# Optimization experiments

Hardware: AMD Instinct MI355X
Metric: run time of the kernel (lower is better)

## Reference

```python
import jax, jax.numpy as jnp
import numpy as np

B, M, HID, NH = 2, 2048, 1024, 16
D = HID // NH  # 64


def setup_inputs() -> dict:
    key = jax.random.key(0)
    ks = jax.random.split(key, 6)
    s = 0.02  # weight init scale
    return {
        "h": jax.random.normal(ks[0], (B, M, HID), dtype=jnp.float32),
        "key_pe": jax.random.normal(ks[1], (1, D, M), dtype=jnp.float32) * s,
        "Wq": jax.random.normal(ks[2], (HID, HID), dtype=jnp.float32) * s,
        "Wk": jax.random.normal(ks[3], (HID, HID), dtype=jnp.float32) * s,
        "Wv": jax.random.normal(ks[4], (HID, HID), dtype=jnp.float32) * s,
        "Wo": jax.random.normal(ks[5], (HID, HID), dtype=jnp.float32) * s,
    }


def reference(h, key_pe, Wq, Wk, Wv, Wo):
    # Faithful to the source: in SelfAttention.forward the gathered-span scores
    # are overwritten by dense Q K^T, and the softmaxed `attn` is discarded;
    # the returned value is (Q K^T) V (no scaling, no softmax). key_pe only
    # feeds the dead softmax branch, so it does not affect the output.
    b, m, hd = h.shape
    nh, d = NH, hd // NH

    def heads(x):  # (B, M, HID) -> (B, NH, M, D)
        return x.reshape(b, m, nh, d).transpose(0, 2, 1, 3)

    q = heads(h @ Wq.T)
    k = heads(h @ Wk.T)
    v = heads(h @ Wv.T)

    attn_cont = jnp.einsum("bhqd,bhkd->bhqk", q, k)  # (B, NH, M, M)
    out = jnp.einsum("bhqk,bhkd->bhqd", attn_cont, v)  # (B, NH, M, D)
    out = out.transpose(0, 2, 1, 3).reshape(b, m, hd)  # (B, M, HID)
    return out @ Wo.T
```

## Files before the change

### kernel.cpp

```cpp
#include <hip/hip_runtime.h>
#include <hip/hip_bf16.h>


typedef unsigned short u16;
typedef unsigned int u32;
typedef __attribute__((ext_vector_type(8))) short bf16x8;
typedef __attribute__((ext_vector_type(4))) float f32x4;

__device__ __forceinline__ void async_copy16(void* lds, const void* g) {
  __builtin_amdgcn_global_load_lds((const __attribute__((address_space(1))) void*)g,
                                   (__attribute__((address_space(3))) void*)lds,
                                   16, 0, 0);
}

__device__ __forceinline__ u16 f2bf(float f) {
  union { __hip_bfloat16 h; u16 u; } c;
  c.h = __float2bfloat16(f);
  return c.u;
}
__device__ __forceinline__ float bflo(u32 w) {
  union { u32 u; float f; } c; c.u = w << 16; return c.f;
}
__device__ __forceinline__ float bfhi(u32 w) {
  union { u32 u; float f; } c; c.u = w & 0xFFFF0000u; return c.f;
}
__device__ __forceinline__ ushort4 cvt4(float4 v) {
  ushort4 o; o.x = f2bf(v.x); o.y = f2bf(v.y); o.z = f2bf(v.z); o.w = f2bf(v.w);
  return o;
}

__global__ __launch_bounds__(256) void prep(const float4* __restrict__ h,
                                            const float4* __restrict__ wq,
                                            const float4* __restrict__ wk,
                                            const float4* __restrict__ wv,
                                            ushort4* __restrict__ hb,
                                            ushort4* __restrict__ wcat) {
  int i = blockIdx.x * 256 + threadIdx.x;
  if (i < 1048576) { hb[i] = cvt4(h[i]); return; }
  i -= 1048576;
  if (i < 262144) { wcat[i] = cvt4(wq[i]); return; }
  i -= 262144;
  if (i < 262144) { wcat[262144 + i] = cvt4(wk[i]); return; }
  i -= 262144;
  wcat[524288 + i] = cvt4(wv[i]);
}

template <bool BF16_OUT>
__global__ __launch_bounds__(256) void gemm_bt(const u16* __restrict__ A, int lda,
                                               const u16* __restrict__ B0,
                                               const u16* __restrict__ B1,
                                               void* __restrict__ Cv,
                                               int N, int K) {
  __shared__ u16 Als[128 * 64];
  __shared__ u16 Bls[128 * 64];
  const int t = threadIdx.x;
  const int lane = t & 63;
  const int wave = t >> 6;
  const int wm = (wave >> 1) * 64;
  const int wn = (wave & 1) * 64;
  const int lrow = lane & 15;
  const int quad = lane >> 4;
  const int m0 = blockIdx.y * 128;
  const int n0 = blockIdx.x * 128;
  const u16* B = (B1 != nullptr && m0 >= 2048) ? B1 : B0;

  const int srow = t >> 3;
  const int scol = (((t & 7) ^ (srow & 7)) * 8);
  const u16* Ag0 = A + (size_t)(m0 + srow) * lda + scol;
  const u16* Bg0 = B + (size_t)(n0 + srow) * K + scol;
  u16* Al0 = Als + t * 8;
  u16* Bl0 = Bls + t * 8;

  f32x4 acc[4][4];
#pragma unroll
  for (int i = 0; i < 4; ++i)
#pragma unroll
    for (int j = 0; j < 4; ++j) acc[i][j] = {0.f, 0.f, 0.f, 0.f};

  for (int k0 = 0; k0 < K; k0 += 64) {
#pragma unroll
    for (int c = 0; c < 4; ++c)
      async_copy16(Al0 + c * 2048, Ag0 + (size_t)(c * 32) * lda + k0);
#pragma unroll
    for (int c = 0; c < 4; ++c)
      async_copy16(Bl0 + c * 2048, Bg0 + (size_t)(c * 32) * K + k0);
    __syncthreads();

#pragma unroll
    for (int half = 0; half < 2; ++half) {
      const int gg = quad + half * 4;
      bf16x8 af[4], bfv[4];
#pragma unroll
      for (int i = 0; i < 4; ++i) {
        const int ra = wm + i * 16 + lrow;
        const int rb = wn + i * 16 + lrow;
        af[i]  = *(const bf16x8*)(Als + ra * 64 + ((gg ^ (ra & 7)) << 3));
        bfv[i] = *(const bf16x8*)(Bls + rb * 64 + ((gg ^ (rb & 7)) << 3));
      }
#pragma unroll
      for (int mi = 0; mi < 4; ++mi)
#pragma unroll
        for (int ni = 0; ni < 4; ++ni)
          acc[mi][ni] = __builtin_amdgcn_mfma_f32_16x16x32_bf16(
              af[mi], bfv[ni], acc[mi][ni], 0, 0, 0);
    }
    __syncthreads();
  }

  const int crow0 = m0 + wm + (lane >> 4) * 4;
  const int ccol0 = n0 + wn + (lane & 15);
#pragma unroll
  for (int mi = 0; mi < 4; ++mi)
#pragma unroll
    for (int ni = 0; ni < 4; ++ni) {
      const int col = ccol0 + ni * 16;
#pragma unroll
      for (int r = 0; r < 4; ++r) {
        const size_t idx = (size_t)(crow0 + mi * 16 + r) * N + col;
        if (BF16_OUT) ((u16*)Cv)[idx]   = f2bf(acc[mi][ni][r]);
        else          ((float*)Cv)[idx] = acc[mi][ni][r];
      }
    }
}

__global__ __launch_bounds__(256) void s_kernel(const u16* __restrict__ QKV,
                                                float* __restrict__ Spart) {
  const int bh = blockIdx.x;
  const int b = bh >> 4, hh = bh & 15;
  const int row0 = b * 2048 + blockIdx.y * 128;
  const u16* Kg = QKV + (size_t)row0 * 3072 + 1024 + hh * 64;

  __shared__ float Ks[64][64];
  __shared__ float Vs[64][64];
  const int t = threadIdx.x;
  const int lr = t >> 2;
  const int lc = (t & 3) * 16;
  const int d1 = (t >> 4) * 4;
  const int d2 = (t & 15) * 4;

  float acc[4][4] = {};

  for (int r0 = 0; r0 < 128; r0 += 64) {
    const u16* kp = Kg + (size_t)(r0 + lr) * 3072 + lc;
    const uint4 kw0 = *(const uint4*)kp;
    const uint4 kw1 = *(const uint4*)(kp + 8);
    const uint4 vw0 = *(const uint4*)(kp + 1024);
    const uint4 vw1 = *(const uint4*)(kp + 1032);
    __syncthreads();
    float* kd = &Ks[lr][lc];
    *(float4*)(kd)      = float4{bflo(kw0.x), bfhi(kw0.x), bflo(kw0.y), bfhi(kw0.y)};
    *(float4*)(kd + 4)  = float4{bflo(kw0.z), bfhi(kw0.z), bflo(kw0.w), bfhi(kw0.w)};
    *(float4*)(kd + 8)  = float4{bflo(kw1.x), bfhi(kw1.x), bflo(kw1.y), bfhi(kw1.y)};
    *(float4*)(kd + 12) = float4{bflo(kw1.z), bfhi(kw1.z), bflo(kw1.w), bfhi(kw1.w)};
    float* vd = &Vs[lr][lc];
    *(float4*)(vd)      = float4{bflo(vw0.x), bfhi(vw0.x), bflo(vw0.y), bfhi(vw0.y)};
    *(float4*)(vd + 4)  = float4{bflo(vw0.z), bfhi(vw0.z), bflo(vw0.w), bfhi(vw0.w)};
    *(float4*)(vd + 8)  = float4{bflo(vw1.x), bfhi(vw1.x), bflo(vw1.y), bfhi(vw1.y)};
    *(float4*)(vd + 12) = float4{bflo(vw1.z), bfhi(vw1.z), bflo(vw1.w), bfhi(vw1.w)};
    __syncthreads();
#pragma unroll
    for (int r = 0; r < 64; ++r) {
      float kv[4], vv[4];
      *(float4*)kv = *(const float4*)&Ks[r][d1];
      *(float4*)vv = *(const float4*)&Vs[r][d2];
#pragma unroll
      for (int i = 0; i < 4; ++i)
#pragma unroll
        for (int j = 0; j < 4; ++j) acc[i][j] += kv[i] * vv[j];
    }
  }
  float* Sp = Spart + ((size_t)bh * 16 + blockIdx.y) * 4096;
#pragma unroll
  for (int i = 0; i < 4; ++i)
    *(float4*)&Sp[(d1 + i) * 64 + d2] =
        float4{acc[i][0], acc[i][1], acc[i][2], acc[i][3]};
}

__global__ __launch_bounds__(256) void reduce_s(const float4* __restrict__ Spart,
                                                float4* __restrict__ S) {
  const int g = blockIdx.x * 256 + threadIdx.x;
  const int bh = g >> 10, j = g & 1023;
  const float4* p = Spart + (size_t)bh * 16384 + j;
  float4 a = {0.f, 0.f, 0.f, 0.f};
#pragma unroll
  for (int c = 0; c < 16; ++c) {
    const float4 v = p[(size_t)c * 1024];
    a.x += v.x; a.y += v.y; a.z += v.z; a.w += v.w;
  }
  S[g] = a;
}

__global__ __launch_bounds__(256) void t_kernel(const float* __restrict__ S,
                                                const float* __restrict__ Wo,
                                                u16* __restrict__ Tt) {
  const int n0 = blockIdx.x * 128;
  const int hh = blockIdx.y;
  const int b  = blockIdx.z;
  __shared__ float Ss[64][68];
  __shared__ float Ws[128][68];
  const int t = threadIdx.x;
  {
    const float* sg = S + (size_t)(b * 16 + hh) * 4096 + (t >> 2) * 64 + (t & 3) * 16;
    float* sd = &Ss[t >> 2][(t & 3) * 16];
#pragma unroll
    for (int i = 0; i < 4; ++i) *(float4*)(sd + 4 * i) = *(const float4*)(sg + 4 * i);
    const float* wg = Wo + (size_t)(n0 + (t >> 1)) * 1024 + hh * 64 + (t & 1) * 32;
    float* wd = &Ws[t >> 1][(t & 1) * 32];
#pragma unroll
    for (int i = 0; i < 8; ++i) *(float4*)(wd + 4 * i) = *(const float4*)(wg + 4 * i);
  }
  __syncthreads();

  const int td = (t >> 4) * 4;
  const int tn = t & 15;
  float acc[4][8] = {};
  for (int jj = 0; jj < 64; jj += 4) {
    float4 sv[4], wv[8];
#pragma unroll
    for (int i = 0; i < 4; ++i) sv[i] = *(const float4*)&Ss[td + i][jj];
#pragma unroll
    for (int k = 0; k < 8; ++k) wv[k] = *(const float4*)&Ws[tn + 16 * k][jj];
#pragma unroll
    for (int i = 0; i < 4; ++i)
#pragma unroll
      for (int k = 0; k < 8; ++k)
        acc[i][k] += sv[i].x * wv[k].x + sv[i].y * wv[k].y +
                     sv[i].z * wv[k].z + sv[i].w * wv[k].w;
  }

  u16* tp = Tt + (size_t)b * 1048576;
#pragma unroll
  for (int k = 0; k < 8; ++k) {
    const int n = n0 + tn + 16 * k;
    ushort4 o;
    o.x = f2bf(acc[0][k]); o.y = f2bf(acc[1][k]);
    o.z = f2bf(acc[2][k]); o.w = f2bf(acc[3][k]);
    *(ushort4*)&tp[(size_t)n * 1024 + hh * 64 + td] = o;
  }
}

extern "C" void kernel_launch(void* const* d_in, const int* in_sizes, int n_in,
                              void* d_out, int out_size, void* d_ws, size_t ws_size,
                              hipStream_t stream) {
  const float* h  = (const float*)d_in[0];
  const float* Wq = (const float*)d_in[2];
  const float* Wk = (const float*)d_in[3];
  const float* Wv = (const float*)d_in[4];
  const float* Wo = (const float*)d_in[5];

  char* ws = (char*)d_ws;
  u16*   hb    = (u16*)(ws);
  u16*   wcat  = (u16*)(ws + (8ull  << 20));
  u16*   QKVb  = (u16*)(ws + (16ull << 20));
  float* S     = (float*)(ws + (40ull << 20));
  u16*   Tt    = (u16*)(ws + (41ull << 20));
  float* Spart = (float*)(ws + (48ull << 20));

  prep<<<7168, 256, 0, stream>>>((const float4*)h, (const float4*)Wq,
                                 (const float4*)Wk, (const float4*)Wv,
                                 (ushort4*)hb, (ushort4*)wcat);
  gemm_bt<true><<<dim3(24, 32), 256, 0, stream>>>(hb, 1024, wcat, nullptr,
                                                  QKVb, 3072, 1024);
  s_kernel<<<dim3(32, 16), 256, 0, stream>>>(QKVb, Spart);
  reduce_s<<<128, 256, 0, stream>>>((const float4*)Spart, (float4*)S);
  t_kernel<<<dim3(8, 16, 2), 256, 0, stream>>>(S, Wo, Tt);
  gemm_bt<false><<<dim3(8, 32), 256, 0, stream>>>(QKVb, 3072, Tt, Tt + 1048576,
                                                  d_out, 1024, 1024);
}
```

Measured before the change: 163.1 us.

## Fold Wq into per-batch output weights instead of projecting Q

```diff
diff --git a/kernel.cpp b/kernel.cpp
--- a/kernel.cpp
+++ b/kernel.cpp
@@ -30,39 +30,68 @@
 }
 
 __global__ __launch_bounds__(256) void prep(const float4* __restrict__ h,
-                                            const float4* __restrict__ wq,
                                             const float4* __restrict__ wk,
                                             const float4* __restrict__ wv,
+                                            const float* __restrict__ wq,
                                             ushort4* __restrict__ hb,
-                                            ushort4* __restrict__ wcat) {
-  int i = blockIdx.x * 256 + threadIdx.x;
-  if (i < 1048576) { hb[i] = cvt4(h[i]); return; }
-  i -= 1048576;
-  if (i < 262144) { wcat[i] = cvt4(wq[i]); return; }
-  i -= 262144;
-  if (i < 262144) { wcat[262144 + i] = cvt4(wk[i]); return; }
-  i -= 262144;
-  wcat[524288 + i] = cvt4(wv[i]);
-}
-
-template <bool BF16_OUT>
+                                            ushort4* __restrict__ wcat2,
+                                            u16* __restrict__ wqt) {
+  __shared__ u16 tile[64][72];
+  const int t = threadIdx.x;
+  if (blockIdx.x < 6144) {
+    int i = blockIdx.x * 256 + t;
+    if (i < 1048576) { hb[i] = cvt4(h[i]); return; }
+    i -= 1048576;
+    if (i < 262144) { wcat2[i] = cvt4(wk[i]); return; }
+    i -= 262144;
+    wcat2[262144 + i] = cvt4(wv[i]);
+    return;
+  }
+  const int tb = blockIdx.x - 6144;
+  const int j0 = (tb >> 4) * 64;
+  const int i0 = (tb & 15) * 64;
+  {
+    const int jr = t >> 2;
+    const int ic = (t & 3) * 16;
+    const float* src = wq + (size_t)(j0 + jr) * 1024 + i0 + ic;
+    u16* dst = &tile[jr][ic];
+#pragma unroll
+    for (int w = 0; w < 4; ++w) {
+      const float4 v = *(const float4*)(src + 4 * w);
+      const ushort4 o = cvt4(v);
+      dst[4 * w] = o.x; dst[4 * w + 1] = o.y; dst[4 * w + 2] = o.z; dst[4 * w + 3] = o.w;
+    }
+  }
+  __syncthreads();
+  {
+    const int ir = t >> 2;
+    const int jc = (t & 3) * 16;
+    u16* dst = wqt + (size_t)(i0 + ir) * 1024 + j0 + jc;
+#pragma unroll
+    for (int w = 0; w < 16; ++w) dst[w] = tile[jc + w][ir];
+  }
+}
+
+template <bool BF16_OUT, int BN>
 __global__ __launch_bounds__(256) void gemm_bt(const u16* __restrict__ A, int lda,
-                                               const u16* __restrict__ B0,
-                                               const u16* __restrict__ B1,
+                                               const u16* __restrict__ B,
                                                void* __restrict__ Cv,
-                                               int N, int K) {
+                                               int N, int K,
+                                               size_t zA, size_t zB, size_t zC) {
+  constexpr int NI = BN / 32;
   __shared__ u16 Als[128 * 64];
-  __shared__ u16 Bls[128 * 64];
+  __shared__ u16 Bls[BN * 64];
   const int t = threadIdx.x;
   const int lane = t & 63;
   const int wave = t >> 6;
   const int wm = (wave >> 1) * 64;
-  const int wn = (wave & 1) * 64;
+  const int wn = (wave & 1) * (BN / 2);
   const int lrow = lane & 15;
   const int quad = lane >> 4;
   const int m0 = blockIdx.y * 128;
-  const int n0 = blockIdx.x * 128;
-  const u16* B = (B1 != nullptr && m0 >= 2048) ? B1 : B0;
+  const int n0 = blockIdx.x * BN;
+  A += (size_t)blockIdx.z * zA;
+  B += (size_t)blockIdx.z * zB;
 
   const int srow = t >> 3;
   const int scol = (((t & 7) ^ (srow & 7)) * 8);
@@ -71,36 +100,39 @@
   u16* Al0 = Als + t * 8;
   u16* Bl0 = Bls + t * 8;
 
-  f32x4 acc[4][4];
+  f32x4 acc[4][NI];
 #pragma unroll
   for (int i = 0; i < 4; ++i)
 #pragma unroll
-    for (int j = 0; j < 4; ++j) acc[i][j] = {0.f, 0.f, 0.f, 0.f};
+    for (int j = 0; j < NI; ++j) acc[i][j] = {0.f, 0.f, 0.f, 0.f};
 
   for (int k0 = 0; k0 < K; k0 += 64) {
 #pragma unroll
     for (int c = 0; c < 4; ++c)
       async_copy16(Al0 + c * 2048, Ag0 + (size_t)(c * 32) * lda + k0);
 #pragma unroll
-    for (int c = 0; c < 4; ++c)
+    for (int c = 0; c < BN / 32; ++c)
       async_copy16(Bl0 + c * 2048, Bg0 + (size_t)(c * 32) * K + k0);
     __syncthreads();
 
 #pragma unroll
     for (int half = 0; half < 2; ++half) {
       const int gg = quad + half * 4;
-      bf16x8 af[4], bfv[4];
+      bf16x8 af[4], bfv[NI];
 #pragma unroll
       for (int i = 0; i < 4; ++i) {
         const int ra = wm + i * 16 + lrow;
+        af[i] = *(const bf16x8*)(Als + ra * 64 + ((gg ^ (ra & 7)) << 3));
+      }
+#pragma unroll
+      for (int i = 0; i < NI; ++i) {
         const int rb = wn + i * 16 + lrow;
-        af[i]  = *(const bf16x8*)(Als + ra * 64 + ((gg ^ (ra & 7)) << 3));
         bfv[i] = *(const bf16x8*)(Bls + rb * 64 + ((gg ^ (rb & 7)) << 3));
       }
 #pragma unroll
       for (int mi = 0; mi < 4; ++mi)
 #pragma unroll
-        for (int ni = 0; ni < 4; ++ni)
+        for (int ni = 0; ni < NI; ++ni)
           acc[mi][ni] = __builtin_amdgcn_mfma_f32_16x16x32_bf16(
               af[mi], bfv[ni], acc[mi][ni], 0, 0, 0);
     }
@@ -112,23 +144,24 @@
 #pragma unroll
   for (int mi = 0; mi < 4; ++mi)
 #pragma unroll
-    for (int ni = 0; ni < 4; ++ni) {
+    for (int ni = 0; ni < NI; ++ni) {
       const int col = ccol0 + ni * 16;
 #pragma unroll
       for (int r = 0; r < 4; ++r) {
-        const size_t idx = (size_t)(crow0 + mi * 16 + r) * N + col;
+        const size_t idx = (size_t)blockIdx.z * zC +
+                           (size_t)(crow0 + mi * 16 + r) * N + col;
         if (BF16_OUT) ((u16*)Cv)[idx]   = f2bf(acc[mi][ni][r]);
         else          ((float*)Cv)[idx] = acc[mi][ni][r];
       }
     }
 }
 
-__global__ __launch_bounds__(256) void s_kernel(const u16* __restrict__ QKV,
+__global__ __launch_bounds__(256) void s_kernel(const u16* __restrict__ KV,
                                                 float* __restrict__ Spart) {
   const int bh = blockIdx.x;
   const int b = bh >> 4, hh = bh & 15;
   const int row0 = b * 2048 + blockIdx.y * 128;
-  const u16* Kg = QKV + (size_t)row0 * 3072 + 1024 + hh * 64;
+  const u16* Kg = KV + (size_t)row0 * 2048 + hh * 64;
 
   __shared__ float Ks[64][64];
   __shared__ float Vs[64][64];
@@ -141,7 +174,7 @@
   float acc[4][4] = {};
 
   for (int r0 = 0; r0 < 128; r0 += 64) {
-    const u16* kp = Kg + (size_t)(r0 + lr) * 3072 + lc;
+    const u16* kp = Kg + (size_t)(r0 + lr) * 2048 + lc;
     const uint4 kw0 = *(const uint4*)kp;
     const uint4 kw1 = *(const uint4*)(kp + 8);
     const uint4 vw0 = *(const uint4*)(kp + 1024);
@@ -250,20 +283,25 @@
 
   char* ws = (char*)d_ws;
   u16*   hb    = (u16*)(ws);
-  u16*   wcat  = (u16*)(ws + (8ull  << 20));
-  u16*   QKVb  = (u16*)(ws + (16ull << 20));
-  float* S     = (float*)(ws + (40ull << 20));
-  u16*   Tt    = (u16*)(ws + (41ull << 20));
-  float* Spart = (float*)(ws + (48ull << 20));
-
-  prep<<<7168, 256, 0, stream>>>((const float4*)h, (const float4*)Wq,
-                                 (const float4*)Wk, (const float4*)Wv,
-                                 (ushort4*)hb, (ushort4*)wcat);
-  gemm_bt<true><<<dim3(24, 32), 256, 0, stream>>>(hb, 1024, wcat, nullptr,
-                                                  QKVb, 3072, 1024);
-  s_kernel<<<dim3(32, 16), 256, 0, stream>>>(QKVb, Spart);
+  u16*   wcat2 = (u16*)(ws + (8ull  << 20));
+  u16*   wqt   = (u16*)(ws + (12ull << 20));
+  u16*   KVb   = (u16*)(ws + (16ull << 20));
+  float* S     = (float*)(ws + (32ull << 20));
+  u16*   Tt    = (u16*)(ws + (33ull << 20));
+  u16*   Ut    = (u16*)(ws + (37ull << 20));
+  float* Spart = (float*)(ws + (41ull << 20));
+
+  prep<<<6400, 256, 0, stream>>>((const float4*)h, (const float4*)Wk,
+                                 (const float4*)Wv, Wq,
+                                 (ushort4*)hb, (ushort4*)wcat2, wqt);
+  gemm_bt<true, 128><<<dim3(16, 32, 1), 256, 0, stream>>>(
+      hb, 1024, wcat2, KVb, 2048, 1024, 0, 0, 0);
+  s_kernel<<<dim3(32, 16), 256, 0, stream>>>(KVb, Spart);
   reduce_s<<<128, 256, 0, stream>>>((const float4*)Spart, (float4*)S);
   t_kernel<<<dim3(8, 16, 2), 256, 0, stream>>>(S, Wo, Tt);
-  gemm_bt<false><<<dim3(8, 32), 256, 0, stream>>>(QKVb, 3072, Tt, Tt + 1048576,
-                                                  d_out, 1024, 1024);
-}
+  gemm_bt<true, 128><<<dim3(8, 8, 2), 256, 0, stream>>>(
+      Tt, 1024, wqt, Ut, 1024, 1024, 1048576, 0, 1048576);
+  gemm_bt<false, 64><<<dim3(16, 16, 2), 256, 0, stream>>>(
+      hb, 1024, Ut, d_out, 1024, 1024,
+      (size_t)2048 * 1024, 1048576, (size_t)2048 * 1024);
+}
```

New measurement: 175.0 us. +7.3%, slower.
